# Kernel optimization log

Hardware: AMD Instinct MI355X
Metric: run time of the kernel (lower is better)

The kernel has to match this reference:

```python
import jax, jax.numpy as jnp
import numpy as np

H = 256
NUM_HEADS = 4
HEAD_DIM = H // NUM_HEADS


def _mlp(x, W1, b1, W2, b2):
    # Linear(2H->H) + ReLU + (dropout=identity in eval) + Linear(H->H)
    h = jax.nn.relu(x @ W1.T + b1)
    return h @ W2.T + b2


def setup_inputs() -> dict:
    key = jax.random.key(0)
    ks = jax.random.split(key, 24)
    s2h = 1.0 / np.sqrt(2 * H)
    sh = 1.0 / np.sqrt(H)
    inp = {
        'qubit_embeddings': jax.random.normal(ks[0], (65536, H), jnp.float32),
        'qpu_embeddings': jax.random.normal(ks[1], (64, H), jnp.float32),
        'gate_embeddings': jax.random.normal(ks[2], (65536, H), jnp.float32),
        'all_embeddings': jax.random.normal(ks[3], (131072, H), jnp.float32),
        'time_table': jax.random.normal(ks[4], (1000, H), jnp.float32),
        'map_W1': jax.random.normal(ks[5], (H, 2 * H), jnp.float32) * s2h,
        'map_b1': jnp.zeros((H,), jnp.float32),
        'map_W2': jax.random.normal(ks[6], (H, H), jnp.float32) * sh,
        'map_b2': jnp.zeros((H,), jnp.float32),
        'sch_W1': jax.random.normal(ks[7], (H, 2 * H), jnp.float32) * s2h,
        'sch_b1': jnp.zeros((H,), jnp.float32),
        'sch_W2': jax.random.normal(ks[8], (H, H), jnp.float32) * sh,
        'sch_b2': jnp.zeros((H,), jnp.float32),
        'qg_W1': jax.random.normal(ks[9], (H, H), jnp.float32) * sh,
        'qg_b1': jnp.zeros((H,), jnp.float32),
        'qg_W2': jax.random.normal(ks[10], (H, H), jnp.float32) * sh,
        'qg_b2': jnp.zeros((H,), jnp.float32),
        'attn_Wq': jax.random.normal(ks[11], (H, H), jnp.float32) * sh,
        'attn_bq': jnp.zeros((H,), jnp.float32),
        'attn_Wk': jax.random.normal(ks[12], (H, H), jnp.float32) * sh,
        'attn_bk': jnp.zeros((H,), jnp.float32),
        'attn_Wv': jax.random.normal(ks[13], (H, H), jnp.float32) * sh,
        'attn_bv': jnp.zeros((H,), jnp.float32),
        'attn_Wo': jax.random.normal(ks[14], (H, H), jnp.float32) * sh,
        'attn_bo': jnp.zeros((H,), jnp.float32),
        'map_qubit': jax.random.randint(ks[15], (131072,), 0, 65536, jnp.int32),
        'map_qpu': jax.random.randint(ks[16], (131072,), 0, 64, jnp.int32),
        'sched_gate': jax.random.randint(ks[17], (131072,), 0, 65536, jnp.int32),
        'sched_time': jax.random.randint(ks[18], (131072,), 0, 1000, jnp.int32),
    }
    return inp


def reference(qubit_embeddings, qpu_embeddings, gate_embeddings, all_embeddings,
              time_table, map_W1, map_b1, map_W2, map_b2,
              sch_W1, sch_b1, sch_W2, sch_b2,
              qg_W1, qg_b1, qg_W2, qg_b2,
              attn_Wq, attn_bq, attn_Wk, attn_bk, attn_Wv, attn_bv,
              attn_Wo, attn_bo,
              map_qubit, map_qpu, sched_gate, sched_time):
    # Vectorized form of the per-action Python loop: gather + concat + MLP.
    map_in = jnp.concatenate([qubit_embeddings[map_qubit], qpu_embeddings[map_qpu]], axis=-1)  # [Nm, 2H]
    map_keys = _mlp(map_in, map_W1, map_b1, map_W2, map_b2)                                    # [Nm, H]
    sch_in = jnp.concatenate([gate_embeddings[sched_gate], time_table[sched_time]], axis=-1)   # [Ns, 2H]
    sch_keys = _mlp(sch_in, sch_W1, sch_b1, sch_W2, sch_b2)                                    # [Ns, H]
    keys = jnp.concatenate([map_keys, sch_keys], axis=0)                                       # [A, H]

    g = all_embeddings.mean(axis=0)                                                            # [H]
    query = jax.nn.relu(g @ qg_W1.T + qg_b1) @ qg_W2.T + qg_b2                                 # [H]

    # MultiheadAttention: batch=1, q_len=1, kv_len=A (dropout=0 in eval, mask all-valid).
    q = (query @ attn_Wq.T + attn_bq).reshape(NUM_HEADS, HEAD_DIM)
    k = (keys @ attn_Wk.T + attn_bk).reshape(-1, NUM_HEADS, HEAD_DIM)
    v = (keys @ attn_Wv.T + attn_bv).reshape(-1, NUM_HEADS, HEAD_DIM)
    scores = jnp.einsum('hd,ahd->ha', q, k) / jnp.sqrt(jnp.asarray(HEAD_DIM, q.dtype))
    w = jax.nn.softmax(scores, axis=-1)                                                        # [heads, A]
    ctx = jnp.einsum('ha,ahd->hd', w, v).reshape(H)
    attn_out = ctx @ attn_Wo.T + attn_bo                                                       # [H]

    action_logits = keys @ attn_out                                                            # [A]
    action_probs = jax.nn.softmax(action_logits, axis=-1)
    return action_probs, action_logits
```

## Files before the change

### kernel.cpp

```cpp
#include <hip/hip_runtime.h>
#include <cstdint>
#include <cstddef>

typedef __bf16 bf16_t;
typedef __bf16 bf16x8 __attribute__((ext_vector_type(8)));
typedef __bf16 bf16x4 __attribute__((ext_vector_type(4)));
typedef __bf16 bf16x2 __attribute__((ext_vector_type(2)));
typedef float f32x4 __attribute__((ext_vector_type(4)));

#define A_TOTAL 262144
#define NMAP    131072

__global__ __launch_bounds__(256) void k_w1b16(
    const float* __restrict__ mW1, const float* __restrict__ sW1,
    bf16_t* __restrict__ dst) {
  int e = blockIdx.x * 256 + threadIdx.x;
  int slice = e >> 16, idx = e & 65535;
  int n = idx >> 8, k = idx & 255;
  float v;
  switch (slice) {
    case 0:  v = mW1[n * 512 + k]; break;
    case 1:  v = mW1[n * 512 + 256 + k]; break;
    case 2:  v = sW1[n * 512 + k]; break;
    default: v = sW1[n * 512 + 256 + k]; break;
  }
  dst[e] = (bf16_t)v;
}

__global__ __launch_bounds__(256) void k_w2ext(
    const float* __restrict__ mW2, const float* __restrict__ sW2,
    bf16_t* __restrict__ wext) {
  int row = blockIdx.x, tab = blockIdx.y, k = threadIdx.x;
  const float* W2 = tab ? sW2 : mW2;
  bf16_t v = (row < 256) ? (bf16_t)W2[row * 256 + k] : (bf16_t)0.f;
  wext[(size_t)tab * 272 * 256 + (size_t)row * 256 + k] = v;
}

__global__ __launch_bounds__(256) void k_mean(const float* __restrict__ A,
                                              float* __restrict__ part) {
  int t = threadIdx.x, b = blockIdx.x;
  const float* base = A + (size_t)b * 512 * 256 + t;
  float s = 0.f;
  for (int r = 0; r < 512; ++r) s += base[(size_t)r * 256];
  part[b * 256 + t] = s;
}

__global__ __launch_bounds__(256) void k_front(
    const float* __restrict__ meanPart,
    const float* __restrict__ qgW1, const float* __restrict__ qgb1,
    const float* __restrict__ qgW2, const float* __restrict__ qgb2,
    const float* __restrict__ Wq,  const float* __restrict__ bq,
    const float* __restrict__ Wk,
    const float* __restrict__ mW2, const float* __restrict__ sW2,
    bf16_t* __restrict__ wext) {
  __shared__ float g[256], h1[256], qry[256], qv[256];
  __shared__ float qks[4][256];
  int t = threadIdx.x;
  float s = 0.f;
  for (int b = 0; b < 256; ++b) s += meanPart[b * 256 + t];
  g[t] = s * (1.0f / 131072.0f);
  __syncthreads();
  {
    const f32x4* row = (const f32x4*)(qgW1 + (size_t)t * 256);
    float acc = 0.f;
    for (int k = 0; k < 64; ++k) {
      f32x4 w = row[k];
      acc += w[0] * g[4 * k] + w[1] * g[4 * k + 1] + w[2] * g[4 * k + 2] + w[3] * g[4 * k + 3];
    }
    h1[t] = fmaxf(acc + qgb1[t], 0.f);
  }
  __syncthreads();
  {
    const f32x4* row = (const f32x4*)(qgW2 + (size_t)t * 256);
    float acc = 0.f;
    for (int k = 0; k < 64; ++k) {
      f32x4 w = row[k];
      acc += w[0] * h1[4 * k] + w[1] * h1[4 * k + 1] + w[2] * h1[4 * k + 2] + w[3] * h1[4 * k + 3];
    }
    qry[t] = acc + qgb2[t];
  }
  __syncthreads();
  {
    const f32x4* row = (const f32x4*)(Wq + (size_t)t * 256);
    float acc = 0.f;
    for (int k = 0; k < 64; ++k) {
      f32x4 w = row[k];
      acc += w[0] * qry[4 * k] + w[1] * qry[4 * k + 1] + w[2] * qry[4 * k + 2] + w[3] * qry[4 * k + 3];
    }
    qv[t] = acc + bq[t];
  }
  __syncthreads();
  for (int h = 0; h < 4; ++h) {
    float acc = 0.f;
    for (int d = 0; d < 64; ++d) acc += qv[h * 64 + d] * Wk[(size_t)(h * 64 + d) * 256 + t];
    qks[h][t] = acc * 0.125f;
  }
  __syncthreads();
  for (int tab = 0; tab < 2; ++tab) {
    const float* W2 = tab ? sW2 : mW2;
    float acc0 = 0.f, acc1 = 0.f, acc2 = 0.f, acc3 = 0.f;
    for (int n = 0; n < 256; ++n) {
      float wv = W2[(size_t)n * 256 + t];
      acc0 += qks[0][n] * wv;
      acc1 += qks[1][n] * wv;
      acc2 += qks[2][n] * wv;
      acc3 += qks[3][n] * wv;
    }
    bf16_t* dst = wext + (size_t)tab * 272 * 256;
    dst[(256 + 0) * 256 + t] = (bf16_t)acc0;
    dst[(256 + 1) * 256 + t] = (bf16_t)acc1;
    dst[(256 + 2) * 256 + t] = (bf16_t)acc2;
    dst[(256 + 3) * 256 + t] = (bf16_t)acc3;
  }
}

__global__ __launch_bounds__(512, 4) void gemm_direct3(
    const float* __restrict__ A0, int M0, const bf16_t* __restrict__ W0,
    const float* __restrict__ b0, bf16_t* __restrict__ C0, int split,
    const float* __restrict__ A1, int M1, const bf16_t* __restrict__ W1,
    const float* __restrict__ b1, bf16_t* __restrict__ C1) {
  __shared__ __align__(16) bf16_t Xo[128][264];
  int blk = blockIdx.x;
  const float* A; int M; const bf16_t* W; const float* bias; bf16_t* C; int bid;
  if (blk < split) { A = A0; M = M0; W = W0; bias = b0; C = C0; bid = blk; }
  else             { A = A1; M = M1; W = W1; bias = b1; C = C1; bid = blk - split; }
  int t = threadIdx.x;
  int w = t >> 6, lane = t & 63;
  int lm = lane & 15, q = lane >> 4;
  int mloc0 = (w & 1) * 64;
  int m0 = bid * 128 + mloc0;
  int c0 = (w >> 1) * 64;
  int rows[4];
#pragma unroll
  for (int i = 0; i < 4; ++i) {
    int m = m0 + i * 16 + lm;
    rows[i] = m < M ? m : M - 1;
  }
  f32x4 acc[4][4] = {};
#pragma unroll
  for (int kt = 0; kt < 8; ++kt) {
    int k0 = kt * 32 + q * 8;
    bf16x8 b[4];
#pragma unroll
    for (int j = 0; j < 4; ++j)
      b[j] = *(const bf16x8*)(W + (size_t)(c0 + j * 16 + lm) * 256 + k0);
#pragma unroll
    for (int i = 0; i < 4; ++i) {
      const float* src = A + (size_t)rows[i] * 256 + k0;
      f32x4 lo = *(const f32x4*)src;
      f32x4 hi = *(const f32x4*)(src + 4);
      bf16x8 a;
#pragma unroll
      for (int x = 0; x < 4; ++x) { a[x] = (bf16_t)lo[x]; a[x + 4] = (bf16_t)hi[x]; }
#pragma unroll
      for (int j = 0; j < 4; ++j)
        acc[i][j] = __builtin_amdgcn_mfma_f32_16x16x32_bf16(a, b[j], acc[i][j], 0, 0, 0);
    }
  }
#pragma unroll
  for (int j = 0; j < 4; ++j) {
    int col = c0 + j * 16 + lm;
    float bb = bias ? bias[col] : 0.f;
#pragma unroll
    for (int i = 0; i < 4; ++i)
#pragma unroll
      for (int r = 0; r < 4; ++r)
        Xo[mloc0 + i * 16 + q * 4 + r][col] = (bf16_t)(acc[i][j][r] + bb);
  }
  __syncthreads();
  size_t tile0 = (size_t)bid * 128;
  const char* lds = (const char*)&Xo[0][0];
#pragma unroll
  for (int s = 0; s < 8; ++s) {
    int flat = s * 8192 + t * 16;
    int row = flat >> 9, colb = flat & 511;
    if (tile0 + (size_t)row < (size_t)M) {
      uint4 v = *(const uint4*)(lds + row * 528 + colb);
      *(uint4*)((char*)C + tile0 * 512 + (size_t)flat) = v;
    }
  }
}

__global__ __launch_bounds__(256, 4) void gemm_gather3(
    const bf16_t* __restrict__ Pa0, const bf16_t* __restrict__ Pb0,
    const int* __restrict__ idxA0, const int* __restrict__ idxB0,
    const bf16_t* __restrict__ Wext0, const float* __restrict__ bias0,
    const bf16_t* __restrict__ Pa1, const bf16_t* __restrict__ Pb1,
    const int* __restrict__ idxA1, const int* __restrict__ idxB1,
    const bf16_t* __restrict__ Wext1, const float* __restrict__ bias1,
    bf16_t* __restrict__ C,
    float* __restrict__ scores, float* __restrict__ partMax) {
  __shared__ __align__(16) bf16_t X[64][264];
  __shared__ float sred[4];
  int blk = blockIdx.x;
  int half = blk >> 11, bid = blk & 2047;
  const bf16_t* Pa; const bf16_t* Pb; const int* idxA; const int* idxB;
  const bf16_t* Wext; const float* bias;
  if (half == 0) { Pa = Pa0; Pb = Pb0; idxA = idxA0; idxB = idxB0; Wext = Wext0; bias = bias0; }
  else           { Pa = Pa1; Pb = Pb1; idxA = idxA1; idxB = idxB1; Wext = Wext1; bias = bias1; }
  int scoreBase = half * NMAP;
  int pmBase = half * 2048;

  int t = threadIdx.x;
  int w = t >> 6, lane = t & 63;
  int lm = lane & 15, q = lane >> 4;
  int cw = w * 64;
  int r = t >> 2, qa = t & 3;
  int row0 = bid * 64;
  int ia = idxA[row0 + r], ib = idxB[row0 + r];
  const bf16_t* paRow = Pa + (size_t)ia * 256;
  const bf16_t* pbRow = Pb + (size_t)ib * 256;

  bf16x8 va[8], vb[8];
#pragma unroll
  for (int s = 0; s < 8; ++s) {
    int ch = s * 4 + qa;
    va[s] = *(const bf16x8*)(paRow + ch * 8);
    vb[s] = *(const bf16x8*)(pbRow + ch * 8);
  }
#pragma unroll
  for (int s = 0; s < 8; ++s) {
    int ch = s * 4 + qa;
    bf16x8 x;
#pragma unroll
    for (int e = 0; e < 8; ++e)
      x[e] = (bf16_t)fmaxf((float)va[s][e] + (float)vb[s][e], 0.f);
    *(bf16x8*)&X[r][ch * 8] = x;
  }
  __syncthreads();

  f32x4 acc[4][4] = {};
  f32x4 accs[4] = {};
  bool doScore = (w == 0);
#pragma unroll
  for (int kt = 0; kt < 8; ++kt) {
    int kl = kt * 32 + q * 8;
    bf16x8 a[4];
#pragma unroll
    for (int i = 0; i < 4; ++i)
      a[i] = *(const bf16x8*)&X[i * 16 + lm][kl];
#pragma unroll
    for (int j = 0; j < 4; ++j) {
      bf16x8 b = *(const bf16x8*)(Wext + (size_t)(cw + j * 16 + lm) * 256 + kl);
#pragma unroll
      for (int i = 0; i < 4; ++i)
        acc[i][j] = __builtin_amdgcn_mfma_f32_16x16x32_bf16(a[i], b, acc[i][j], 0, 0, 0);
    }
    if (doScore) {
      bf16x8 bs = *(const bf16x8*)(Wext + (size_t)(256 + lm) * 256 + kl);
#pragma unroll
      for (int i = 0; i < 4; ++i)
        accs[i] = __builtin_amdgcn_mfma_f32_16x16x32_bf16(a[i], bs, accs[i], 0, 0, 0);
    }
  }
  __syncthreads();
#pragma unroll
  for (int j = 0; j < 4; ++j) {
    int col = cw + j * 16 + lm;
    float bb = bias[col];
#pragma unroll
    for (int i = 0; i < 4; ++i)
#pragma unroll
      for (int rr = 0; rr < 4; ++rr)
        X[i * 16 + q * 4 + rr][col] = (bf16_t)(acc[i][j][rr] + bb);
  }
  float hmax = -3.4e38f;
  if (doScore) {
    if (lm < 4) {
#pragma unroll
      for (int i = 0; i < 4; ++i)
#pragma unroll
        for (int rr = 0; rr < 4; ++rr) {
          int m = i * 16 + q * 4 + rr;
          float v = accs[i][rr];
          scores[(size_t)lm * A_TOTAL + scoreBase + row0 + m] = v;
          hmax = fmaxf(hmax, v);
        }
    }
    float m1 = fmaxf(hmax, __shfl_xor(hmax, 16));
    float m2 = fmaxf(m1, __shfl_xor(m1, 32));
    if (lane < 4) sred[lane] = m2;
  }
  __syncthreads();
  size_t gRow0 = (size_t)(half * NMAP + row0);
  const char* lds = (const char*)&X[0][0];
#pragma unroll
  for (int s = 0; s < 8; ++s) {
    int flat = s * 4096 + t * 16;
    int row = flat >> 9, colb = flat & 511;
    uint4 v = *(const uint4*)(lds + row * 528 + colb);
    *(uint4*)((char*)C + gRow0 * 512 + (size_t)flat) = v;
  }
  if (t < 4) partMax[t * 4096 + pmBase + bid] = sred[t];
}

__global__ __launch_bounds__(256) void k_smax2(const float* __restrict__ pM,
                                               float* __restrict__ Mh) {
  int t = threadIdx.x;
  __shared__ float red[256];
  for (int h = 0; h < 4; ++h) {
    float m = -3.4e38f;
    for (int i = t; i < 4096; i += 256) m = fmaxf(m, pM[h * 4096 + i]);
    red[t] = m;
    __syncthreads();
    for (int s = 128; s > 0; s >>= 1) {
      if (t < s) red[t] = fmaxf(red[t], red[t + s]);
      __syncthreads();
    }
    if (t == 0) Mh[h] = red[0];
    __syncthreads();
  }
}

__global__ __launch_bounds__(256) void k_ssum(const float* __restrict__ scores,
                                              const float* __restrict__ Mh,
                                              float* __restrict__ part) {
  int b = blockIdx.x, t = threadIdx.x;
  float m = Mh[b >> 6];
  const float* base = scores + (size_t)b * 4096;
  float s = 0.f;
  for (int i = 0; i < 16; ++i) s += __expf(base[i * 256 + t] - m);
  __shared__ float red[256];
  red[t] = s;
  __syncthreads();
  for (int st = 128; st > 0; st >>= 1) {
    if (t < st) red[t] += red[t + st];
    __syncthreads();
  }
  if (t == 0) part[b] = red[0];
}

__global__ __launch_bounds__(256) void k_ssum2(const float* __restrict__ part,
                                               float* __restrict__ invS) {
  int t = threadIdx.x;
  __shared__ float red[256];
  red[t] = part[t];
  __syncthreads();
  for (int s = 32; s > 0; s >>= 1) {
    if ((t & 63) < s) red[t] += red[t + s];
    __syncthreads();
  }
  if ((t & 63) == 0) invS[t >> 6] = 1.0f / red[t];
}

__global__ __launch_bounds__(256) void k_u(
    const bf16_t* __restrict__ keys, const float* __restrict__ scores,
    const float* __restrict__ Mh, const float* __restrict__ invS,
    float* __restrict__ u) {
  __shared__ float wl[4][512];
  __shared__ float uloc[8][4][256];
  int t = threadIdx.x;
  int a0 = blockIdx.x * 512;
#pragma unroll
  for (int i = 0; i < 8; ++i) {
    int e = i * 256 + t;
    int h = e >> 9, rr = e & 511;
    wl[h][rr] = __expf(scores[(size_t)h * A_TOTAL + a0 + rr] - Mh[h]) * invS[h];
  }
  __syncthreads();
  int tc = t & 31, rh = t >> 5;
  float acc[4][8] = {};
  for (int rr = 0; rr < 64; ++rr) {
    int al = rh * 64 + rr;
    bf16x8 kv = *(const bf16x8*)(keys + (size_t)(a0 + al) * 256 + tc * 8);
    float f[8];
#pragma unroll
    for (int e = 0; e < 8; ++e) f[e] = (float)kv[e];
#pragma unroll
    for (int h = 0; h < 4; ++h) {
      float wv = wl[h][al];
#pragma unroll
      for (int e = 0; e < 8; ++e) acc[h][e] += wv * f[e];
    }
  }
#pragma unroll
  for (int h = 0; h < 4; ++h)
#pragma unroll
    for (int e = 0; e < 8; ++e) uloc[rh][h][tc * 8 + e] = acc[h][e];
  __syncthreads();
#pragma unroll
  for (int h = 0; h < 4; ++h) {
    float v = 0.f;
#pragma unroll
    for (int g = 0; g < 8; ++g) v += uloc[g][h][t];
    atomicAdd(&u[h * 256 + t], v);
  }
}

__global__ __launch_bounds__(256) void k_attn(
    const float* __restrict__ u, const float* __restrict__ Wv,
    const float* __restrict__ bv, const float* __restrict__ Wo,
    const float* __restrict__ bo, float* __restrict__ attn_out,
    bf16_t* __restrict__ attn_pad) {
  __shared__ float ctx[256];
  int t = threadIdx.x;
  int h = t >> 6;
  const float* uh = u + h * 256;
  {
    const f32x4* row = (const f32x4*)(Wv + (size_t)t * 256);
    float acc = 0.f;
    for (int k = 0; k < 64; ++k) {
      f32x4 w = row[k];
      acc += w[0] * uh[4 * k] + w[1] * uh[4 * k + 1] + w[2] * uh[4 * k + 2] + w[3] * uh[4 * k + 3];
    }
    ctx[t] = acc + bv[t];
  }
  __syncthreads();
  {
    const f32x4* row = (const f32x4*)(Wo + (size_t)t * 256);
    float acc = 0.f;
    for (int k = 0; k < 64; ++k) {
      f32x4 w = row[k];
      acc += w[0] * ctx[4 * k] + w[1] * ctx[4 * k + 1] + w[2] * ctx[4 * k + 2] + w[3] * ctx[4 * k + 3];
    }
    float v = acc + bo[t];
    attn_out[t] = v;
    attn_pad[t] = (bf16_t)v;
#pragma unroll
    for (int i = 1; i < 16; ++i) attn_pad[i * 256 + t] = (bf16_t)0.f;
  }
}

__global__ __launch_bounds__(256) void k_logits2(
    const bf16_t* __restrict__ keys, const bf16_t* __restrict__ attn_pad,
    float* __restrict__ out_logits, float* __restrict__ blockMax) {
  int t = threadIdx.x;
  int w = t >> 6, lane = t & 63;
  int lm = lane & 15, q = lane >> 4;
  int m0 = blockIdx.x * 256 + w * 64;
  bf16x8 b[8];
#pragma unroll
  for (int kt = 0; kt < 8; ++kt)
    b[kt] = *(const bf16x8*)(attn_pad + lm * 256 + kt * 32 + q * 8);
  f32x4 acc[4] = {};
#pragma unroll
  for (int i = 0; i < 4; ++i) {
    const bf16_t* arow = keys + (size_t)(m0 + i * 16 + lm) * 256 + q * 8;
#pragma unroll
    for (int kt = 0; kt < 8; ++kt) {
      bf16x8 a = *(const bf16x8*)(arow + kt * 32);
      acc[i] = __builtin_amdgcn_mfma_f32_16x16x32_bf16(a, b[kt], acc[i], 0, 0, 0);
    }
  }
  float lmax = -3.4e38f;
  if (lm == 0) {
#pragma unroll
    for (int i = 0; i < 4; ++i) {
      *(f32x4*)(out_logits + m0 + i * 16 + q * 4) = acc[i];
#pragma unroll
      for (int rr = 0; rr < 4; ++rr) lmax = fmaxf(lmax, acc[i][rr]);
    }
  }
  float m1 = fmaxf(lmax, __shfl_xor(lmax, 16));
  float m2 = fmaxf(m1, __shfl_xor(m1, 32));
  __shared__ float red[4];
  if (lane == 0) red[w] = m2;
  __syncthreads();
  if (t == 0)
    blockMax[blockIdx.x] = fmaxf(fmaxf(red[0], red[1]), fmaxf(red[2], red[3]));
}

__global__ __launch_bounds__(256) void k_lred1(const float* __restrict__ bm,
                                               float* __restrict__ Ml) {
  int t = threadIdx.x;
  float m = -3.4e38f;
  for (int i = t; i < 1024; i += 256) m = fmaxf(m, bm[i]);
  __shared__ float red[256];
  red[t] = m;
  __syncthreads();
  for (int s = 128; s > 0; s >>= 1) {
    if (t < s) red[t] = fmaxf(red[t], red[t + s]);
    __syncthreads();
  }
  if (t == 0) Ml[0] = red[0];
}

__global__ __launch_bounds__(256) void k_lsum(const float* __restrict__ logits,
                                              const float* __restrict__ Ml,
                                              float* __restrict__ part) {
  int t = threadIdx.x, b = blockIdx.x;
  float m = Ml[0];
  float s = __expf(logits[b * 512 + t] - m) + __expf(logits[b * 512 + 256 + t] - m);
  __shared__ float red[256];
  red[t] = s;
  __syncthreads();
  for (int st = 128; st > 0; st >>= 1) {
    if (t < st) red[t] += red[t + st];
    __syncthreads();
  }
  if (t == 0) part[b] = red[0];
}

__global__ __launch_bounds__(256) void k_lred2(const float* __restrict__ part,
                                               float* __restrict__ invSl) {
  int t = threadIdx.x;
  float s = part[t] + part[t + 256];
  __shared__ float red[256];
  red[t] = s;
  __syncthreads();
  for (int st = 128; st > 0; st >>= 1) {
    if (t < st) red[t] += red[t + st];
    __syncthreads();
  }
  if (t == 0) invSl[0] = 1.0f / red[0];
}

__global__ __launch_bounds__(256) void k_probs(const float* __restrict__ logits,
                                               const float* __restrict__ Ml,
                                               const float* __restrict__ invSl,
                                               float* __restrict__ probs) {
  int i = blockIdx.x * 256 + threadIdx.x;
  probs[i] = __expf(logits[i] - Ml[0]) * invSl[0];
}

extern "C" void kernel_launch(void* const* d_in, const int* in_sizes, int n_in,
                              void* d_out, int out_size, void* d_ws, size_t ws_size,
                              hipStream_t stream) {
  const float* qubit_emb = (const float*)d_in[0];
  const float* qpu_emb   = (const float*)d_in[1];
  const float* gate_emb  = (const float*)d_in[2];
  const float* all_emb   = (const float*)d_in[3];
  const float* time_tab  = (const float*)d_in[4];
  const float* map_W1 = (const float*)d_in[5];
  const float* map_b1 = (const float*)d_in[6];
  const float* map_W2 = (const float*)d_in[7];
  const float* map_b2 = (const float*)d_in[8];
  const float* sch_W1 = (const float*)d_in[9];
  const float* sch_b1 = (const float*)d_in[10];
  const float* sch_W2 = (const float*)d_in[11];
  const float* sch_b2 = (const float*)d_in[12];
  const float* qg_W1 = (const float*)d_in[13];
  const float* qg_b1 = (const float*)d_in[14];
  const float* qg_W2 = (const float*)d_in[15];
  const float* qg_b2 = (const float*)d_in[16];
  const float* Wq = (const float*)d_in[17];
  const float* bq = (const float*)d_in[18];
  const float* Wk = (const float*)d_in[19];
  const float* Wv = (const float*)d_in[21];
  const float* bv = (const float*)d_in[22];
  const float* Wo = (const float*)d_in[23];
  const float* bo = (const float*)d_in[24];
  const int* map_qubit  = (const int*)d_in[25];
  const int* map_qpu    = (const int*)d_in[26];
  const int* sched_gate = (const int*)d_in[27];
  const int* sched_time = (const int*)d_in[28];
  (void)in_sizes; (void)n_in; (void)out_size;

  char* ws = (char*)d_ws;
  size_t off = 0;
  auto alloc = [&](size_t b) { size_t r = off; off += (b + 255) & ~(size_t)255; return r; };
  size_t KEYS  = alloc((size_t)A_TOTAL * 256 * 2);
  size_t PQ    = alloc((size_t)65536 * 256 * 2);
  size_t PG    = alloc((size_t)65536 * 256 * 2);
  size_t PP    = alloc((size_t)128 * 256 * 2);
  size_t PT    = alloc((size_t)1024 * 256 * 2);
  size_t W1B   = alloc((size_t)4 * 65536 * 2);
  size_t WEXT  = alloc((size_t)2 * 272 * 256 * 2);
  size_t SCORE = alloc((size_t)4 * A_TOTAL * 4);
  size_t MPART = alloc((size_t)256 * 256 * 4);
  size_t APAD  = alloc((size_t)16 * 256 * 2);
  size_t ATTN  = alloc(256 * 4);
  size_t U     = alloc(4 * 256 * 4);
  size_t PMAX  = alloc(4 * 4096 * 4);
  size_t MH    = alloc(4 * 4);
  size_t SINV  = alloc(4 * 4);
  size_t BMAX  = alloc(1024 * 4);
  size_t ML    = alloc(4);
  size_t SLINV = alloc(4);
  size_t LPART = alloc(512 * 4);
  size_t SPART = alloc(256 * 4);
  if (off > ws_size) return;

  bf16_t* keysP  = (bf16_t*)(ws + KEYS);
  bf16_t* pqP    = (bf16_t*)(ws + PQ);
  bf16_t* pgP    = (bf16_t*)(ws + PG);
  bf16_t* ppP    = (bf16_t*)(ws + PP);
  bf16_t* ptP    = (bf16_t*)(ws + PT);
  bf16_t* w1bP   = (bf16_t*)(ws + W1B);
  bf16_t* wextP  = (bf16_t*)(ws + WEXT);
  float*  scoreP = (float*)(ws + SCORE);
  float*  mpartP = (float*)(ws + MPART);
  bf16_t* apadP  = (bf16_t*)(ws + APAD);
  float*  attnP  = (float*)(ws + ATTN);
  float*  uP     = (float*)(ws + U);
  float*  pmaxP  = (float*)(ws + PMAX);
  float*  mhP    = (float*)(ws + MH);
  float*  sinvP  = (float*)(ws + SINV);
  float*  bmaxP  = (float*)(ws + BMAX);
  float*  mlP    = (float*)(ws + ML);
  float*  slinvP = (float*)(ws + SLINV);
  float*  lpartP = (float*)(ws + LPART);
  float*  spartP = (float*)(ws + SPART);

  float* probsOut  = (float*)d_out;
  float* logitsOut = probsOut + A_TOTAL;

  hipMemsetAsync(uP, 0, 4 * 256 * 4, stream);

  k_w1b16<<<1024, 256, 0, stream>>>(map_W1, sch_W1, w1bP);
  k_w2ext<<<dim3(272, 2), 256, 0, stream>>>(map_W2, sch_W2, wextP);
  k_mean<<<256, 256, 0, stream>>>(all_emb, mpartP);
  k_front<<<1, 256, 0, stream>>>(mpartP, qg_W1, qg_b1, qg_W2, qg_b2,
                                 Wq, bq, Wk, map_W2, sch_W2, wextP);

  gemm_direct3<<<1024, 512, 0, stream>>>(
      qubit_emb, 65536, w1bP + 0 * 65536, nullptr, pqP, 512,
      gate_emb,  65536, w1bP + 2 * 65536, nullptr, pgP);
  gemm_direct3<<<9, 512, 0, stream>>>(
      qpu_emb, 64,   w1bP + 1 * 65536, map_b1, ppP, 1,
      time_tab, 1000, w1bP + 3 * 65536, sch_b1, ptP);

  gemm_gather3<<<4096, 256, 0, stream>>>(
      pqP, ppP, map_qubit, map_qpu, wextP, map_b2,
      pgP, ptP, sched_gate, sched_time, wextP + 272 * 256, sch_b2,
      keysP, scoreP, pmaxP);

  k_smax2<<<1, 256, 0, stream>>>(pmaxP, mhP);
  k_ssum<<<256, 256, 0, stream>>>(scoreP, mhP, spartP);
  k_ssum2<<<1, 256, 0, stream>>>(spartP, sinvP);

  k_u<<<512, 256, 0, stream>>>(keysP, scoreP, mhP, sinvP, uP);
  k_attn<<<1, 256, 0, stream>>>(uP, Wv, bv, Wo, bo, attnP, apadP);

  k_logits2<<<1024, 256, 0, stream>>>(keysP, apadP, logitsOut, bmaxP);
  k_lred1<<<1, 256, 0, stream>>>(bmaxP, mlP);
  k_lsum<<<512, 256, 0, stream>>>(logitsOut, mlP, lpartP);
  k_lred2<<<1, 256, 0, stream>>>(lpartP, slinvP);
  k_probs<<<1024, 256, 0, stream>>>(logitsOut, mlP, slinvP, probsOut);
}
```

Measured before the change: 754.6 us.

## Eliminate second MLP layer GEMM by folding W2 into attention and logit vectors

Stops materializing the keys (second-layer MLP output) and instead stores the hidden activation X after ReLU. Every use of keys is linear: scores, the weighted value sum and the logits. So W2 and b2 are folded into the query-side vectors. Scores come from dot products of X with precomputed qW vectors, the weighted sum of X is projected through W2 in a tiny kernel, and the logits use X times W2ᵀ·attn plus a bias constant. This removes the big 262144×256×256 MFMA GEMM, at the cost of extra small single-block kernels and some changed rounding order.

```diff
diff --git a/kernel.cpp b/kernel.cpp
--- a/kernel.cpp
+++ b/kernel.cpp
@@ -5,7 +5,6 @@
 typedef __bf16 bf16_t;
 typedef __bf16 bf16x8 __attribute__((ext_vector_type(8)));
 typedef __bf16 bf16x4 __attribute__((ext_vector_type(4)));
-typedef __bf16 bf16x2 __attribute__((ext_vector_type(2)));
 typedef float f32x4 __attribute__((ext_vector_type(4)));
 
 #define A_TOTAL 262144
@@ -27,15 +26,6 @@
   dst[e] = (bf16_t)v;
 }
 
-__global__ __launch_bounds__(256) void k_w2ext(
-    const float* __restrict__ mW2, const float* __restrict__ sW2,
-    bf16_t* __restrict__ wext) {
-  int row = blockIdx.x, tab = blockIdx.y, k = threadIdx.x;
-  const float* W2 = tab ? sW2 : mW2;
-  bf16_t v = (row < 256) ? (bf16_t)W2[row * 256 + k] : (bf16_t)0.f;
-  wext[(size_t)tab * 272 * 256 + (size_t)row * 256 + k] = v;
-}
-
 __global__ __launch_bounds__(256) void k_mean(const float* __restrict__ A,
                                               float* __restrict__ part) {
   int t = threadIdx.x, b = blockIdx.x;
@@ -52,7 +42,7 @@
     const float* __restrict__ Wq,  const float* __restrict__ bq,
     const float* __restrict__ Wk,
     const float* __restrict__ mW2, const float* __restrict__ sW2,
-    bf16_t* __restrict__ wext) {
+    float* __restrict__ qw) {
   __shared__ float g[256], h1[256], qry[256], qv[256];
   __shared__ float qks[4][256];
   int t = threadIdx.x;
@@ -106,11 +96,11 @@
       acc2 += qks[2][n] * wv;
       acc3 += qks[3][n] * wv;
     }
-    bf16_t* dst = wext + (size_t)tab * 272 * 256;
-    dst[(256 + 0) * 256 + t] = (bf16_t)acc0;
-    dst[(256 + 1) * 256 + t] = (bf16_t)acc1;
-    dst[(256 + 2) * 256 + t] = (bf16_t)acc2;
-    dst[(256 + 3) * 256 + t] = (bf16_t)acc3;
+    float* dst = qw + tab * 1024;
+    dst[0 * 256 + t] = acc0;
+    dst[1 * 256 + t] = acc1;
+    dst[2 * 256 + t] = acc2;
+    dst[3 * 256 + t] = acc3;
   }
 }
 
@@ -181,117 +171,77 @@
   }
 }
 
-__global__ __launch_bounds__(256, 4) void gemm_gather3(
+__global__ __launch_bounds__(256) void k_gx(
     const bf16_t* __restrict__ Pa0, const bf16_t* __restrict__ Pb0,
     const int* __restrict__ idxA0, const int* __restrict__ idxB0,
-    const bf16_t* __restrict__ Wext0, const float* __restrict__ bias0,
     const bf16_t* __restrict__ Pa1, const bf16_t* __restrict__ Pb1,
     const int* __restrict__ idxA1, const int* __restrict__ idxB1,
-    const bf16_t* __restrict__ Wext1, const float* __restrict__ bias1,
-    bf16_t* __restrict__ C,
-    float* __restrict__ scores, float* __restrict__ partMax) {
-  __shared__ __align__(16) bf16_t X[64][264];
-  __shared__ float sred[4];
-  int blk = blockIdx.x;
-  int half = blk >> 11, bid = blk & 2047;
-  const bf16_t* Pa; const bf16_t* Pb; const int* idxA; const int* idxB;
-  const bf16_t* Wext; const float* bias;
-  if (half == 0) { Pa = Pa0; Pb = Pb0; idxA = idxA0; idxB = idxB0; Wext = Wext0; bias = bias0; }
-  else           { Pa = Pa1; Pb = Pb1; idxA = idxA1; idxB = idxB1; Wext = Wext1; bias = bias1; }
-  int scoreBase = half * NMAP;
-  int pmBase = half * 2048;
-
-  int t = threadIdx.x;
-  int w = t >> 6, lane = t & 63;
-  int lm = lane & 15, q = lane >> 4;
-  int cw = w * 64;
-  int r = t >> 2, qa = t & 3;
-  int row0 = bid * 64;
-  int ia = idxA[row0 + r], ib = idxB[row0 + r];
-  const bf16_t* paRow = Pa + (size_t)ia * 256;
-  const bf16_t* pbRow = Pb + (size_t)ib * 256;
-
-  bf16x8 va[8], vb[8];
-#pragma unroll
-  for (int s = 0; s < 8; ++s) {
-    int ch = s * 4 + qa;
-    va[s] = *(const bf16x8*)(paRow + ch * 8);
-    vb[s] = *(const bf16x8*)(pbRow + ch * 8);
-  }
-#pragma unroll
-  for (int s = 0; s < 8; ++s) {
-    int ch = s * 4 + qa;
-    bf16x8 x;
-#pragma unroll
-    for (int e = 0; e < 8; ++e)
-      x[e] = (bf16_t)fmaxf((float)va[s][e] + (float)vb[s][e], 0.f);
-    *(bf16x8*)&X[r][ch * 8] = x;
-  }
-  __syncthreads();
-
-  f32x4 acc[4][4] = {};
-  f32x4 accs[4] = {};
-  bool doScore = (w == 0);
-#pragma unroll
-  for (int kt = 0; kt < 8; ++kt) {
-    int kl = kt * 32 + q * 8;
-    bf16x8 a[4];
-#pragma unroll
-    for (int i = 0; i < 4; ++i)
-      a[i] = *(const bf16x8*)&X[i * 16 + lm][kl];
-#pragma unroll
-    for (int j = 0; j < 4; ++j) {
-      bf16x8 b = *(const bf16x8*)(Wext + (size_t)(cw + j * 16 + lm) * 256 + kl);
-#pragma unroll
-      for (int i = 0; i < 4; ++i)
-        acc[i][j] = __builtin_amdgcn_mfma_f32_16x16x32_bf16(a[i], b, acc[i][j], 0, 0, 0);
-    }
-    if (doScore) {
-      bf16x8 bs = *(const bf16x8*)(Wext + (size_t)(256 + lm) * 256 + kl);
-#pragma unroll
-      for (int i = 0; i < 4; ++i)
-        accs[i] = __builtin_amdgcn_mfma_f32_16x16x32_bf16(a[i], bs, accs[i], 0, 0, 0);
-    }
-  }
-  __syncthreads();
-#pragma unroll
-  for (int j = 0; j < 4; ++j) {
-    int col = cw + j * 16 + lm;
-    float bb = bias[col];
-#pragma unroll
-    for (int i = 0; i < 4; ++i)
-#pragma unroll
-      for (int rr = 0; rr < 4; ++rr)
-        X[i * 16 + q * 4 + rr][col] = (bf16_t)(acc[i][j][rr] + bb);
-  }
-  float hmax = -3.4e38f;
-  if (doScore) {
-    if (lm < 4) {
-#pragma unroll
-      for (int i = 0; i < 4; ++i)
-#pragma unroll
-        for (int rr = 0; rr < 4; ++rr) {
-          int m = i * 16 + q * 4 + rr;
-          float v = accs[i][rr];
-          scores[(size_t)lm * A_TOTAL + scoreBase + row0 + m] = v;
-          hmax = fmaxf(hmax, v);
-        }
-    }
-    float m1 = fmaxf(hmax, __shfl_xor(hmax, 16));
-    float m2 = fmaxf(m1, __shfl_xor(m1, 32));
-    if (lane < 4) sred[lane] = m2;
-  }
-  __syncthreads();
-  size_t gRow0 = (size_t)(half * NMAP + row0);
-  const char* lds = (const char*)&X[0][0];
-#pragma unroll
-  for (int s = 0; s < 8; ++s) {
-    int flat = s * 4096 + t * 16;
-    int row = flat >> 9, colb = flat & 511;
-    uint4 v = *(const uint4*)(lds + row * 528 + colb);
-    *(uint4*)((char*)C + gRow0 * 512 + (size_t)flat) = v;
-  }
-  if (t < 4) partMax[t * 4096 + pmBase + bid] = sred[t];
+    const float* __restrict__ qw,
+    bf16_t* __restrict__ X, float* __restrict__ scores,
+    float* __restrict__ partMax) {
+  __shared__ float qs[4][256];
+  __shared__ float sc[4][64];
+  int t = threadIdx.x;
+  int b = blockIdx.x;
+  int rows0 = b * 64;
+  int half = rows0 >= NMAP ? 1 : 0;
+  const bf16_t* Pa = half ? Pa1 : Pa0;
+  const bf16_t* Pb = half ? Pb1 : Pb0;
+  const int* idxA = half ? idxA1 : idxA0;
+  const int* idxB = half ? idxB1 : idxB0;
+  int lrow0 = rows0 - half * NMAP;
+
+  {
+    f32x4 v = *(const f32x4*)(qw + half * 1024 + t * 4);
+    *(f32x4*)&((float*)qs)[t * 4] = v;
+  }
+
+  int rg = t >> 5;
+  int cl = t & 31;
+  int ia[8], ib[8];
+#pragma unroll
+  for (int it = 0; it < 8; ++it) {
+    ia[it] = idxA[lrow0 + it * 8 + rg];
+    ib[it] = idxB[lrow0 + it * 8 + rg];
+  }
+  __syncthreads();
+
+#pragma unroll
+  for (int it = 0; it < 8; ++it) {
+    int rowg = it * 8 + rg;
+    bf16x8 a8 = *(const bf16x8*)(Pa + (size_t)ia[it] * 256 + cl * 8);
+    bf16x8 b8 = *(const bf16x8*)(Pb + (size_t)ib[it] * 256 + cl * 8);
+    float x[8];
+    bf16x8 xo;
+#pragma unroll
+    for (int e = 0; e < 8; ++e) {
+      x[e] = fmaxf((float)a8[e] + (float)b8[e], 0.f);
+      xo[e] = (bf16_t)x[e];
+    }
+    *(bf16x8*)(X + (size_t)(rows0 + rowg) * 256 + cl * 8) = xo;
+    float p[4] = {0.f, 0.f, 0.f, 0.f};
+#pragma unroll
+    for (int h = 0; h < 4; ++h)
+#pragma unroll
+      for (int e = 0; e < 8; ++e)
+        p[h] += x[e] * qs[h][cl * 8 + e];
+#pragma unroll
+    for (int h = 0; h < 4; ++h) {
+#pragma unroll
+      for (int o = 16; o > 0; o >>= 1) p[h] += __shfl_xor(p[h], o);
+      if (cl == 0) sc[h][rowg] = p[h];
+    }
+  }
+  __syncthreads();
+  {
+    int h = t >> 6, l = t & 63;
+    float v = sc[h][l];
+    scores[(size_t)h * A_TOTAL + rows0 + l] = v;
+    float m = v;
+#pragma unroll
+    for (int o = 32; o > 0; o >>= 1) m = fmaxf(m, __shfl_xor(m, o));
+    if (l == 0) partMax[h * 4096 + b] = m;
+  }
 }
 
 __global__ __launch_bounds__(256) void k_smax2(const float* __restrict__ pM,
@@ -343,14 +293,15 @@
   if ((t & 63) == 0) invS[t >> 6] = 1.0f / red[t];
 }
 
-__global__ __launch_bounds__(256) void k_u(
-    const bf16_t* __restrict__ keys, const float* __restrict__ scores,
+__global__ __launch_bounds__(256) void k_u3(
+    const bf16_t* __restrict__ X, const float* __restrict__ scores,
     const float* __restrict__ Mh, const float* __restrict__ invS,
-    float* __restrict__ u) {
+    float* __restrict__ y, float* __restrict__ shalf) {
   __shared__ float wl[4][512];
   __shared__ float uloc[8][4][256];
   int t = threadIdx.x;
   int a0 = blockIdx.x * 512;
+  int half = blockIdx.x >> 8;
 #pragma unroll
   for (int i = 0; i < 8; ++i) {
     int e = i * 256 + t;
@@ -358,11 +309,20 @@
     wl[h][rr] = __expf(scores[(size_t)h * A_TOTAL + a0 + rr] - Mh[h]) * invS[h];
   }
   __syncthreads();
+  {
+    int h = t >> 6, l = t & 63;
+    float s = 0.f;
+#pragma unroll
+    for (int j = 0; j < 8; ++j) s += wl[h][l + j * 64];
+#pragma unroll
+    for (int o = 32; o > 0; o >>= 1) s += __shfl_xor(s, o);
+    if (l == 0) atomicAdd(&shalf[half * 4 + h], s);
+  }
   int tc = t & 31, rh = t >> 5;
   float acc[4][8] = {};
   for (int rr = 0; rr < 64; ++rr) {
     int al = rh * 64 + rr;
-    bf16x8 kv = *(const bf16x8*)(keys + (size_t)(a0 + al) * 256 + tc * 8);
+    bf16x8 kv = *(const bf16x8*)(X + (size_t)(a0 + al) * 256 + tc * 8);
     float f[8];
 #pragma unroll
     for (int e = 0; e < 8; ++e) f[e] = (float)kv[e];
@@ -383,59 +343,125 @@
     float v = 0.f;
 #pragma unroll
     for (int g = 0; g < 8; ++g) v += uloc[g][h][t];
-    atomicAdd(&u[h * 256 + t], v);
-  }
-}
-
-__global__ __launch_bounds__(256) void k_attn(
-    const float* __restrict__ u, const float* __restrict__ Wv,
-    const float* __restrict__ bv, const float* __restrict__ Wo,
-    const float* __restrict__ bo, float* __restrict__ attn_out,
-    bf16_t* __restrict__ attn_pad) {
+    atomicAdd(&y[(half * 4 + h) * 256 + t], v);
+  }
+}
+
+__global__ __launch_bounds__(256) void k_attn2(
+    const float* __restrict__ y,
+    const float* __restrict__ shalf,
+    const float* __restrict__ mW2, const float* __restrict__ sW2,
+    const float* __restrict__ mb2, const float* __restrict__ sb2,
+    const float* __restrict__ Wv, const float* __restrict__ bv,
+    const float* __restrict__ Wo, const float* __restrict__ bo,
+    float* __restrict__ attnv, float* __restrict__ c01) {
+  __shared__ float ys[2][4][256];
+  __shared__ float us[4][256];
   __shared__ float ctx[256];
-  int t = threadIdx.x;
-  int h = t >> 6;
-  const float* uh = u + h * 256;
-  {
+  __shared__ float att[256];
+  __shared__ float r0[4], r1[4];
+  int t = threadIdx.x;
+#pragma unroll
+  for (int i = 0; i < 8; ++i) ((float*)ys)[i * 256 + t] = y[i * 256 + t];
+  __syncthreads();
+  {
+    int j = t;
+    float a0 = 0.f, a1 = 0.f, a2 = 0.f, a3 = 0.f;
+    const f32x4* rm = (const f32x4*)(mW2 + (size_t)j * 256);
+    const f32x4* rs = (const f32x4*)(sW2 + (size_t)j * 256);
+    for (int k = 0; k < 64; ++k) {
+      f32x4 wm = rm[k], wsv = rs[k];
+#pragma unroll
+      for (int e = 0; e < 4; ++e) {
+        float w0 = wm[e], w1 = wsv[e];
+        int kk = k * 4 + e;
+        a0 += ys[0][0][kk] * w0 + ys[1][0][kk] * w1;
+        a1 += ys[0][1][kk] * w0 + ys[1][1][kk] * w1;
+        a2 += ys[0][2][kk] * w0 + ys[1][2][kk] * w1;
+        a3 += ys[0][3][kk] * w0 + ys[1][3][kk] * w1;
+      }
+    }
+    float bm = mb2[j], bs = sb2[j];
+    us[0][j] = a0 + shalf[0] * bm + shalf[4] * bs;
+    us[1][j] = a1 + shalf[1] * bm + shalf[5] * bs;
+    us[2][j] = a2 + shalf[2] * bm + shalf[6] * bs;
+    us[3][j] = a3 + shalf[3] * bm + shalf[7] * bs;
+  }
+  __syncthreads();
+  {
+    int h = t >> 6;
     const f32x4* row = (const f32x4*)(Wv + (size_t)t * 256);
+    const f32x4* uh = (const f32x4*)us[h];
     float acc = 0.f;
     for (int k = 0; k < 64; ++k) {
-      f32x4 w = row[k];
-      acc += w[0] * uh[4 * k] + w[1] * uh[4 * k + 1] + w[2] * uh[4 * k + 2] + w[3] * uh[4 * k + 3];
+      f32x4 w = row[k], x = uh[k];
+      acc += w[0] * x[0] + w[1] * x[1] + w[2] * x[2] + w[3] * x[3];
     }
     ctx[t] = acc + bv[t];
   }
   __syncthreads();
   {
     const f32x4* row = (const f32x4*)(Wo + (size_t)t * 256);
+    const f32x4* cx = (const f32x4*)ctx;
     float acc = 0.f;
     for (int k = 0; k < 64; ++k) {
-      f32x4 w = row[k];
-      acc += w[0] * ctx[4 * k] + w[1] * ctx[4 * k + 1] + w[2] * ctx[4 * k + 2] + w[3] * ctx[4 * k + 3];
+      f32x4 w = row[k], x = cx[k];
+      acc += w[0] * x[0] + w[1] * x[1] + w[2] * x[2] + w[3] * x[3];
     }
     float v = acc + bo[t];
-    attn_out[t] = v;
-    attn_pad[t] = (bf16_t)v;
-#pragma unroll
-    for (int i = 1; i < 16; ++i) attn_pad[i * 256 + t] = (bf16_t)0.f;
-  }
-}
-
-__global__ __launch_bounds__(256) void k_logits2(
-    const bf16_t* __restrict__ keys, const bf16_t* __restrict__ attn_pad,
+    att[t] = v;
+    attnv[t] = v;
+  }
+  __syncthreads();
+  {
+    float p0 = mb2[t] * att[t], p1 = sb2[t] * att[t];
+#pragma unroll
+    for (int o = 32; o > 0; o >>= 1) {
+      p0 += __shfl_xor(p0, o);
+      p1 += __shfl_xor(p1, o);
+    }
+    if ((t & 63) == 0) { r0[t >> 6] = p0; r1[t >> 6] = p1; }
+    __syncthreads();
+    if (t == 0) c01[0] = r0[0] + r0[1] + r0[2] + r0[3];
+    if (t == 1) c01[1] = r1[0] + r1[1] + r1[2] + r1[3];
+  }
+}
+
+__global__ __launch_bounds__(256) void k_zc(
+    const float* __restrict__ mW2, const float* __restrict__ sW2,
+    const float* __restrict__ attnv, bf16_t* __restrict__ zpad) {
+  int tab = blockIdx.x, t = threadIdx.x;
+  const float* W2 = tab ? sW2 : mW2;
+  __shared__ float att[256];
+  att[t] = attnv[t];
+  __syncthreads();
+  float acc = 0.f;
+  for (int j = 0; j < 256; ++j) acc += W2[(size_t)j * 256 + t] * att[j];
+  bf16_t* dst = zpad + (size_t)tab * 16 * 256;
+  dst[t] = (bf16_t)acc;
+#pragma unroll
+  for (int i = 1; i < 16; ++i) dst[i * 256 + t] = (bf16_t)0.f;
+}
+
+__global__ __launch_bounds__(256) void k_logits3(
+    const bf16_t* __restrict__ X, const bf16_t* __restrict__ zpad,
+    const float* __restrict__ c01,
     float* __restrict__ out_logits, float* __restrict__ blockMax) {
   int t = threadIdx.x;
   int w = t >> 6, lane = t & 63;
   int lm = lane & 15, q = lane >> 4;
+  int half = blockIdx.x >> 9;
+  float c = c01[half];
   int m0 = blockIdx.x * 256 + w * 64;
+  const bf16_t* zp = zpad + (size_t)half * 16 * 256;
   bf16x8 b[8];
 #pragma unroll
   for (int kt = 0; kt < 8; ++kt)
-    b[kt] = *(const bf16x8*)(attn_pad + lm * 256 + kt * 32 + q * 8);
+    b[kt] = *(const bf16x8*)(zp + lm * 256 + kt * 32 + q * 8);
   f32x4 acc[4] = {};
 #pragma unroll
   for (int i = 0; i < 4; ++i) {
-    const bf16_t* arow = keys + (size_t)(m0 + i * 16 + lm) * 256 + q * 8;
+    const bf16_t* arow = X + (size_t)(m0 + i * 16 + lm) * 256 + q * 8;
 #pragma unroll
     for (int kt = 0; kt < 8; ++kt) {
       bf16x8 a = *(const bf16x8*)(arow + kt * 32);
@@ -446,9 +472,14 @@
   if (lm == 0) {
 #pragma unroll
     for (int i = 0; i < 4; ++i) {
-      *(f32x4*)(out_logits + m0 + i * 16 + q * 4) = acc[i];
-#pragma unroll
-      for (int rr = 0; rr < 4; ++rr) lmax = fmaxf(lmax, acc[i][rr]);
+      f32x4 v4;
+#pragma unroll
+      for (int rr = 0; rr < 4; ++rr) {
+        float v = acc[i][rr] + c;
+        v4[rr] = v;
+        lmax = fmaxf(lmax, v);
+      }
+      *(f32x4*)(out_logits + m0 + i * 16 + q * 4) = v4;
     }
   }
   float m1 = fmaxf(lmax, __shfl_xor(lmax, 16));
@@ -549,18 +580,20 @@
   char* ws = (char*)d_ws;
   size_t off = 0;
   auto alloc = [&](size_t b) { size_t r = off; off += (b + 255) & ~(size_t)255; return r; };
-  size_t KEYS  = alloc((size_t)A_TOTAL * 256 * 2);
+  size_t XB    = alloc((size_t)A_TOTAL * 256 * 2);
   size_t PQ    = alloc((size_t)65536 * 256 * 2);
   size_t PG    = alloc((size_t)65536 * 256 * 2);
   size_t PP    = alloc((size_t)128 * 256 * 2);
   size_t PT    = alloc((size_t)1024 * 256 * 2);
   size_t W1B   = alloc((size_t)4 * 65536 * 2);
-  size_t WEXT  = alloc((size_t)2 * 272 * 256 * 2);
+  size_t QW    = alloc((size_t)2 * 4 * 256 * 4);
   size_t SCORE = alloc((size_t)4 * A_TOTAL * 4);
   size_t MPART = alloc((size_t)256 * 256 * 4);
-  size_t APAD  = alloc((size_t)16 * 256 * 2);
-  size_t ATTN  = alloc(256 * 4);
-  size_t U     = alloc(4 * 256 * 4);
+  size_t ZPAD  = alloc((size_t)2 * 16 * 256 * 2);
+  size_t ATTNV = alloc(256 * 4);
+  size_t Y     = alloc(2 * 4 * 256 * 4);
+  size_t SH    = alloc(2 * 4 * 4);
+  size_t C01   = alloc(2 * 4);
   size_t PMAX  = alloc(4 * 4096 * 4);
   size_t MH    = alloc(4 * 4);
   size_t SINV  = alloc(4 * 4);
@@ -571,18 +604,20 @@
   size_t SPART = alloc(256 * 4);
   if (off > ws_size) return;
 
-  bf16_t* keysP  = (bf16_t*)(ws + KEYS);
+  bf16_t* xP     = (bf16_t*)(ws + XB);
   bf16_t* pqP    = (bf16_t*)(ws + PQ);
   bf16_t* pgP    = (bf16_t*)(ws + PG);
   bf16_t* ppP    = (bf16_t*)(ws + PP);
   bf16_t* ptP    = (bf16_t*)(ws + PT);
   bf16_t* w1bP   = (bf16_t*)(ws + W1B);
-  bf16_t* wextP  = (bf16_t*)(ws + WEXT);
+  float*  qwP    = (float*)(ws + QW);
   float*  scoreP = (float*)(ws + SCORE);
   float*  mpartP = (float*)(ws + MPART);
-  bf16_t* apadP  = (bf16_t*)(ws + APAD);
-  float*  attnP  = (float*)(ws + ATTN);
-  float*  uP     = (float*)(ws + U);
+  bf16_t* zpadP  = (bf16_t*)(ws + ZPAD);
+  float*  attnvP = (float*)(ws + ATTNV);
+  float*  yP     = (float*)(ws + Y);
+  float*  shP    = (float*)(ws + SH);
+  float*  c01P   = (float*)(ws + C01);
   float*  pmaxP  = (float*)(ws + PMAX);
   float*  mhP    = (float*)(ws + MH);
   float*  sinvP  = (float*)(ws + SINV);
@@ -595,13 +630,12 @@
   float* probsOut  = (float*)d_out;
   float* logitsOut = probsOut + A_TOTAL;
 
-  hipMemsetAsync(uP, 0, 4 * 256 * 4, stream);
+  hipMemsetAsync(yP, 0, 8448, stream);
 
   k_w1b16<<<1024, 256, 0, stream>>>(map_W1, sch_W1, w1bP);
-  k_w2ext<<<dim3(272, 2), 256, 0, stream>>>(map_W2, sch_W2, wextP);
   k_mean<<<256, 256, 0, stream>>>(all_emb, mpartP);
   k_front<<<1, 256, 0, stream>>>(mpartP, qg_W1, qg_b1, qg_W2, qg_b2,
-                                 Wq, bq, Wk, map_W2, sch_W2, wextP);
+                                 Wq, bq, Wk, map_W2, sch_W2, qwP);
 
   gemm_direct3<<<1024, 512, 0, stream>>>(
       qubit_emb, 65536, w1bP + 0 * 65536, nullptr, pqP, 512,
@@ -610,19 +644,21 @@
       qpu_emb, 64,   w1bP + 1 * 65536, map_b1, ppP, 1,
       time_tab, 1000, w1bP + 3 * 65536, sch_b1, ptP);
 
-  gemm_gather3<<<4096, 256, 0, stream>>>(
-      pqP, ppP, map_qubit, map_qpu, wextP, map_b2,
-      pgP, ptP, sched_gate, sched_time, wextP + 272 * 256, sch_b2,
-      keysP, scoreP, pmaxP);
+  k_gx<<<4096, 256, 0, stream>>>(
+      pqP, ppP, map_qubit, map_qpu,
+      pgP, ptP, sched_gate, sched_time,
+      qwP, xP, scoreP, pmaxP);
 
   k_smax2<<<1, 256, 0, stream>>>(pmaxP, mhP);
   k_ssum<<<256, 256, 0, stream>>>(scoreP, mhP, spartP);
   k_ssum2<<<1, 256, 0, stream>>>(spartP, sinvP);
 
-  k_u<<<512, 256, 0, stream>>>(keysP, scoreP, mhP, sinvP, uP);
-  k_attn<<<1, 256, 0, stream>>>(uP, Wv, bv, Wo, bo, attnP, apadP);
-
-  k_logits2<<<1024, 256, 0, stream>>>(keysP, apadP, logitsOut, bmaxP);
+  k_u3<<<512, 256, 0, stream>>>(xP, scoreP, mhP, sinvP, yP, shP);
+  k_attn2<<<1, 256, 0, stream>>>(yP, shP, map_W2, sch_W2, map_b2, sch_b2,
+                                 Wv, bv, Wo, bo, attnvP, c01P);
+  k_zc<<<2, 256, 0, stream>>>(map_W2, sch_W2, attnvP, zpadP);
+
+  k_logits3<<<1024, 256, 0, stream>>>(xP, zpadP, c01P, logitsOut, bmaxP);
   k_lred1<<<1, 256, 0, stream>>>(bmaxP, mlP);
   k_lsum<<<512, 256, 0, stream>>>(logitsOut, mlP, lpartP);
   k_lred2<<<1, 256, 0, stream>>>(lpartP, slinvP);
```

Measured after the change: 717.1 us. 5.0% less time.
